# Kernel optimization log

Hardware: AMD Instinct MI355X
Metric: run time of the kernel (lower is better)

The kernel has to match this reference:

```python
import jax, jax.numpy as jnp
import numpy as np

N_NODES = 100000
N_EDGES = 1600000
F_IN = 128
F_OUT = 64


def setup_inputs() -> dict:
    key = jax.random.key(0)
    k0, k1, k2, k3, k4, k5 = jax.random.split(key, 6)
    stdv = 1.0 / np.sqrt(F_OUT)
    x = jax.random.normal(k0, (N_NODES, F_IN), dtype=jnp.float32)
    edge_src = jax.random.randint(k1, (N_EDGES,), 0, N_NODES, dtype=jnp.int32)
    edge_dst = jax.random.randint(k2, (N_EDGES,), 0, N_NODES, dtype=jnp.int32)
    # normalized adjacency values (all positive, like D^-1/2 A D^-1/2 entries)
    edge_weight = jax.random.uniform(k3, (N_EDGES,), dtype=jnp.float32)
    weight = jax.random.uniform(k4, (F_IN, F_OUT), dtype=jnp.float32, minval=-stdv, maxval=stdv)
    bias = jax.random.uniform(k5, (F_OUT,), dtype=jnp.float32, minval=-stdv, maxval=stdv)
    return {"x": x, "edge_weight": edge_weight, "weight": weight, "bias": bias,
            "edge_src": edge_src, "edge_dst": edge_dst}


def reference(x, edge_weight, weight, bias, edge_src, edge_dst):
    # support = X @ W  -- dense GEMM [N, F_in] x [F_in, F_out]
    support = x @ weight
    # spmm(adj, support): adj in COO form; gather source rows, scale by edge value,
    # scatter-add into destination rows.
    msgs = support[edge_src] * edge_weight[:, None]          # [E, F_out]
    out = jax.ops.segment_sum(msgs, edge_dst, num_segments=x.shape[0])
    return out + bias
```

## Files before the change

### kernel.cpp

```cpp
#include <hip/hip_runtime.h>
#include <hip/hip_bf16.h>

#define F_IN 128
#define F_OUT 64
#define BUCKET_SHIFT 7
#define BUCKET_NODES 128
#define BUCKET_CAP 2880
#define CNT_STRIDE 16
#define NB_MAX 800
#define SCAT_CHUNK 8192
#define GEMM_ROWS 64
#define LDK 136

typedef __attribute__((ext_vector_type(8))) short bf16x8;
typedef __attribute__((ext_vector_type(4))) float f32x4;

__device__ inline short bf16_bits(float f) {
  __hip_bfloat16 h = __float2bfloat16(f);
  return *reinterpret_cast<short*>(&h);
}

__global__ __launch_bounds__(256) void gcn_gemm_mfma_kernel(
    const float* __restrict__ x, const float* __restrict__ w,
    __hip_bfloat16* __restrict__ support, int n_nodes) {
  __shared__ short As[GEMM_ROWS][LDK];
  __shared__ short Bs[F_OUT][LDK];
  const int tid = threadIdx.x;
  const int block_row = blockIdx.x * GEMM_ROWS;

#pragma unroll
  for (int i = 0; i < F_IN * F_OUT / 256; ++i) {
    const int idx = tid + i * 256;
    const int k = idx >> 6;
    const int n = idx & 63;
    Bs[n][k] = bf16_bits(w[idx]);
  }
#pragma unroll
  for (int i = 0; i < GEMM_ROWS * F_IN / 4 / 256; ++i) {
    const int idx = tid + i * 256;
    const int row = idx >> 5;
    const int c4 = idx & 31;
    float4 v = make_float4(0.f, 0.f, 0.f, 0.f);
    if (block_row + row < n_nodes)
      v = ((const float4*)(x + (size_t)(block_row + row) * F_IN))[c4];
    short4 b;
    b.x = bf16_bits(v.x);
    b.y = bf16_bits(v.y);
    b.z = bf16_bits(v.z);
    b.w = bf16_bits(v.w);
    *(short4*)&As[row][c4 * 4] = b;
  }
  __syncthreads();

  const int lane = tid & 63;
  const int wid = tid >> 6;
  const int wr0 = wid * 16;
  const int m = lane & 15;
  const int quad = lane >> 4;

  f32x4 acc0 = {0.f, 0.f, 0.f, 0.f};
  f32x4 acc1 = {0.f, 0.f, 0.f, 0.f};
  f32x4 acc2 = {0.f, 0.f, 0.f, 0.f};
  f32x4 acc3 = {0.f, 0.f, 0.f, 0.f};
#pragma unroll
  for (int ks = 0; ks < 4; ++ks) {
    const int ko = ks * 32 + quad * 8;
    const bf16x8 a  = *(const bf16x8*)&As[wr0 + m][ko];
    const bf16x8 b0 = *(const bf16x8*)&Bs[0 + m][ko];
    const bf16x8 b1 = *(const bf16x8*)&Bs[16 + m][ko];
    const bf16x8 b2 = *(const bf16x8*)&Bs[32 + m][ko];
    const bf16x8 b3 = *(const bf16x8*)&Bs[48 + m][ko];
    acc0 = __builtin_amdgcn_mfma_f32_16x16x32_bf16(a, b0, acc0, 0, 0, 0);
    acc1 = __builtin_amdgcn_mfma_f32_16x16x32_bf16(a, b1, acc1, 0, 0, 0);
    acc2 = __builtin_amdgcn_mfma_f32_16x16x32_bf16(a, b2, acc2, 0, 0, 0);
    acc3 = __builtin_amdgcn_mfma_f32_16x16x32_bf16(a, b3, acc3, 0, 0, 0);
  }
#pragma unroll
  for (int r = 0; r < 4; ++r) {
    const int row = block_row + wr0 + quad * 4 + r;
    if (row < n_nodes) {
      __hip_bfloat16* op = support + (size_t)row * F_OUT;
      op[0 + m]  = __float2bfloat16(acc0[r]);
      op[16 + m] = __float2bfloat16(acc1[r]);
      op[32 + m] = __float2bfloat16(acc2[r]);
      op[48 + m] = __float2bfloat16(acc3[r]);
    }
  }
}

__global__ __launch_bounds__(512) void gcn_bucket_scatter_kernel(
    const int* __restrict__ esrc, const int* __restrict__ edst,
    const float* __restrict__ ew, int* __restrict__ bcount,
    int2* __restrict__ region, int n_edges, int nb) {
  __shared__ int lhist[NB_MAX];
  __shared__ int lcur[NB_MAX];
  __shared__ int ldst_cache[SCAT_CHUNK];
  const int e0 = blockIdx.x * SCAT_CHUNK;
  const int e1 = min(e0 + SCAT_CHUNK, n_edges);
  const int n_local = e1 - e0;

  for (int i = threadIdx.x; i < nb; i += 512) lhist[i] = 0;
  __syncthreads();
  for (int i = threadIdx.x; i < n_local; i += 512) {
    const int d = edst[e0 + i];
    ldst_cache[i] = d;
    atomicAdd(&lhist[d >> BUCKET_SHIFT], 1);
  }
  __syncthreads();
  for (int b = threadIdx.x; b < nb; b += 512) {
    const int c = lhist[b];
    lcur[b] = c ? atomicAdd(&bcount[b * CNT_STRIDE], c) : 0;
  }
  __syncthreads();
  for (int i = threadIdx.x; i < n_local; i += 512) {
    const int d = ldst_cache[i];
    const int b = d >> BUCKET_SHIFT;
    const int pos = atomicAdd(&lcur[b], 1);
    if (pos < BUCKET_CAP) {
      region[(size_t)b * BUCKET_CAP + pos] =
          make_int2((esrc[e0 + i] << BUCKET_SHIFT) | (d & (BUCKET_NODES - 1)),
                    __float_as_int(ew[e0 + i]));
    }
  }
}

__global__ __launch_bounds__(1024) void gcn_bucket_scan_kernel(
    const int* __restrict__ bcount, int* __restrict__ bbase, int nb) {
  __shared__ int wtot[16];
  const int lane = threadIdx.x & 63;
  const int wid = threadIdx.x >> 6;
  int c = 0;
  if (threadIdx.x < nb) {
    c = bcount[threadIdx.x * CNT_STRIDE];
    c = (c < BUCKET_CAP ? c : BUCKET_CAP);
  }
  int s = c;
#pragma unroll
  for (int off = 1; off < 64; off <<= 1) {
    const int t = __shfl_up(s, off, 64);
    if (lane >= off) s += t;
  }
  if (lane == 63) wtot[wid] = s;
  __syncthreads();
  if (wid == 0) {
    const int wv = (lane < 16) ? wtot[lane] : 0;
    int wsc = wv;
#pragma unroll
    for (int off = 1; off < 16; off <<= 1) {
      const int t = __shfl_up(wsc, off, 64);
      if (lane >= off) wsc += t;
    }
    if (lane < 16) wtot[lane] = wsc - wv;
  }
  __syncthreads();
  if (threadIdx.x < nb) bbase[threadIdx.x] = (s - c) + wtot[wid];
}

__global__ __launch_bounds__(256) void gcn_bucket_sort_kernel(
    const int2* __restrict__ region, const int* __restrict__ bcount,
    const int* __restrict__ bbase, int2* __restrict__ sorted,
    int* __restrict__ ends, int n_nodes) {
  __shared__ int2 eb[BUCKET_CAP];
  __shared__ int2 outb[BUCKET_CAP];
  __shared__ int lhist[BUCKET_NODES];
  __shared__ int lcur[BUCKET_NODES];
  const int b = blockIdx.x;
  int cnt = bcount[b * CNT_STRIDE];
  cnt = (cnt < BUCKET_CAP ? cnt : BUCKET_CAP);
  const int gbase = bbase[b];
  const int node0 = b << BUCKET_SHIFT;

  for (int i = threadIdx.x; i < BUCKET_NODES; i += 256) lhist[i] = 0;
  __syncthreads();
  for (int i = threadIdx.x; i < cnt; i += 256) {
    const int2 p = region[(size_t)b * BUCKET_CAP + i];
    eb[i] = p;
    atomicAdd(&lhist[p.x & (BUCKET_NODES - 1)], 1);
  }
  __syncthreads();
  const int lane = threadIdx.x & 63;
  if (threadIdx.x < 64) {
    const int v0 = lhist[lane];
    const int v1 = lhist[64 + lane];
    int s0 = v0;
#pragma unroll
    for (int off = 1; off < 64; off <<= 1) {
      const int t = __shfl_up(s0, off, 64);
      if (lane >= off) s0 += t;
    }
    const int tot0 = __shfl(s0, 63, 64);
    int s1 = v1;
#pragma unroll
    for (int off = 1; off < 64; off <<= 1) {
      const int t = __shfl_up(s1, off, 64);
      if (lane >= off) s1 += t;
    }
    s1 += tot0;
    lcur[lane] = s0 - v0;
    lcur[64 + lane] = s1 - v1;
    const int n0 = node0 + lane;
    const int n1 = node0 + 64 + lane;
    if (n0 < n_nodes) ends[n0] = gbase + s0;
    if (n1 < n_nodes) ends[n1] = gbase + s1;
  }
  __syncthreads();
  for (int i = threadIdx.x; i < cnt; i += 256) {
    const int2 p = eb[i];
    const int ldst = p.x & (BUCKET_NODES - 1);
    const int pos = atomicAdd(&lcur[ldst], 1);
    outb[pos] = make_int2(p.x >> BUCKET_SHIFT, p.y);
  }
  __syncthreads();
  for (int i = threadIdx.x; i < cnt; i += 256) {
    sorted[gbase + i] = outb[i];
  }
}

__global__ __launch_bounds__(256) void gcn_aggregate_kernel(
    const __hip_bfloat16* __restrict__ support, const int2* __restrict__ sorted,
    const int* __restrict__ ends, const float* __restrict__ bias,
    float* __restrict__ out, int n_nodes) {
  const int node = (blockIdx.x * 256 + threadIdx.x) >> 6;
  const int lane = threadIdx.x & 63;
  if (node >= n_nodes) return;
  const int start = (node == 0) ? 0 : ends[node - 1];
  const int end = ends[node];
  float acc = 0.f;
  for (int base = start; base < end; base += 64) {
    const int m = end - base;
    int2 meta = make_int2(0, 0);
    if (lane < m) meta = sorted[base + lane];
    const int m4 = (m < 64 ? m : 64);
    const int mr = (m4 + 7) & ~7;
    for (int j = 0; j < mr; j += 8) {
      int sidx[8];
      float wv[8];
#pragma unroll
      for (int u = 0; u < 8; ++u) {
        sidx[u] = __shfl(meta.x, j + u, 64);
        wv[u] = __int_as_float(__shfl(meta.y, j + u, 64));
      }
      float v[8];
#pragma unroll
      for (int u = 0; u < 8; ++u)
        v[u] = __bfloat162float(support[(size_t)sidx[u] * F_OUT + lane]);
#pragma unroll
      for (int u = 0; u < 8; ++u) acc += v[u] * wv[u];
    }
  }
  out[(size_t)node * F_OUT + lane] = acc + bias[lane];
}

extern "C" void kernel_launch(void* const* d_in, const int* in_sizes, int n_in,
                              void* d_out, int out_size, void* d_ws, size_t ws_size,
                              hipStream_t stream) {
  const float* x    = (const float*)d_in[0];
  const float* ew   = (const float*)d_in[1];
  const float* w    = (const float*)d_in[2];
  const float* bias = (const float*)d_in[3];
  const int*   esrc = (const int*)d_in[4];
  const int*   edst = (const int*)d_in[5];
  float* out = (float*)d_out;

  const int n_nodes = in_sizes[0] / F_IN;
  const int n_edges = in_sizes[4];
  const int nb = (n_nodes + BUCKET_NODES - 1) >> BUCKET_SHIFT;

  char* ws = (char*)d_ws;
  int2* sorted = (int2*)ws;
  ws += ((size_t)n_edges * sizeof(int2) + 255) / 256 * 256;
  int* ends = (int*)ws;
  ws += ((size_t)n_nodes * sizeof(int) + 255) / 256 * 256;
  int* bcount = (int*)ws;
  const size_t bcount_bytes = (size_t)nb * CNT_STRIDE * sizeof(int);
  ws += (bcount_bytes + 255) / 256 * 256;
  int* bbase = (int*)ws;
  ws += ((size_t)nb * sizeof(int) + 255) / 256 * 256;
  int2* region = (int2*)ws;
  __hip_bfloat16* support = (__hip_bfloat16*)ws;

  hipMemsetAsync(bcount, 0, bcount_bytes, stream);
  gcn_bucket_scatter_kernel<<<(n_edges + SCAT_CHUNK - 1) / SCAT_CHUNK, 512, 0,
                              stream>>>(esrc, edst, ew, bcount, region, n_edges,
                                        nb);
  gcn_bucket_scan_kernel<<<1, 1024, 0, stream>>>(bcount, bbase, nb);
  gcn_bucket_sort_kernel<<<nb, 256, 0, stream>>>(region, bcount, bbase, sorted,
                                                 ends, n_nodes);
  gcn_gemm_mfma_kernel<<<(n_nodes + GEMM_ROWS - 1) / GEMM_ROWS, 256, 0,
                         stream>>>(x, w, support, n_nodes);
  gcn_aggregate_kernel<<<(n_nodes * 64 + 255) / 256, 256, 0, stream>>>(
      support, sorted, ends, bias, out, n_nodes);
}
```

Measured before the change: 198.4 us.

## Fuse GEMM with bucket scatter, fold scan into sort, vectorize aggregate gathers

Merges the bucket-scatter and bf16 MFMA GEMM into one heterogeneous launch, with blocks branching on their id and sharing LDS through a union. GEMM tiles grow to 128 rows with 512 threads. The separate single-block scan kernel is removed, and each sort block now sums the counts of the preceding buckets itself. The aggregate kernel has each lane load 4 bf16 values for one of four edges at a time, then combines lanes with a cross-lane reduction and writes float4 outputs. This cuts launch count and serialization and uses wider gathers, at the cost of redundant prefix work in the sort and needing separate workspace for support when space allows.

```diff
diff --git a/kernel.cpp b/kernel.cpp
--- a/kernel.cpp
+++ b/kernel.cpp
@@ -9,7 +9,7 @@
 #define CNT_STRIDE 16
 #define NB_MAX 800
 #define SCAT_CHUNK 8192
-#define GEMM_ROWS 64
+#define P1_GEMM_ROWS 128
 #define LDK 136
 
 typedef __attribute__((ext_vector_type(8))) short bf16x8;
@@ -20,165 +20,146 @@
   return *reinterpret_cast<short*>(&h);
 }
 
-__global__ __launch_bounds__(256) void gcn_gemm_mfma_kernel(
+union Phase1Smem {
+  struct { short As[P1_GEMM_ROWS][LDK]; short Bs[F_OUT][LDK]; } g;
+  struct { int lhist[NB_MAX]; int lcur[NB_MAX]; int ldst[SCAT_CHUNK]; } s;
+};
+
+__global__ __launch_bounds__(512, 6) void gcn_phase1_kernel(
     const float* __restrict__ x, const float* __restrict__ w,
-    __hip_bfloat16* __restrict__ support, int n_nodes) {
-  __shared__ short As[GEMM_ROWS][LDK];
-  __shared__ short Bs[F_OUT][LDK];
-  const int tid = threadIdx.x;
-  const int block_row = blockIdx.x * GEMM_ROWS;
-
-#pragma unroll
-  for (int i = 0; i < F_IN * F_OUT / 256; ++i) {
-    const int idx = tid + i * 256;
-    const int k = idx >> 6;
-    const int n = idx & 63;
-    Bs[n][k] = bf16_bits(w[idx]);
-  }
-#pragma unroll
-  for (int i = 0; i < GEMM_ROWS * F_IN / 4 / 256; ++i) {
-    const int idx = tid + i * 256;
-    const int row = idx >> 5;
-    const int c4 = idx & 31;
-    float4 v = make_float4(0.f, 0.f, 0.f, 0.f);
-    if (block_row + row < n_nodes)
-      v = ((const float4*)(x + (size_t)(block_row + row) * F_IN))[c4];
-    short4 b;
-    b.x = bf16_bits(v.x);
-    b.y = bf16_bits(v.y);
-    b.z = bf16_bits(v.z);
-    b.w = bf16_bits(v.w);
-    *(short4*)&As[row][c4 * 4] = b;
-  }
-  __syncthreads();
-
-  const int lane = tid & 63;
-  const int wid = tid >> 6;
-  const int wr0 = wid * 16;
-  const int m = lane & 15;
-  const int quad = lane >> 4;
-
-  f32x4 acc0 = {0.f, 0.f, 0.f, 0.f};
-  f32x4 acc1 = {0.f, 0.f, 0.f, 0.f};
-  f32x4 acc2 = {0.f, 0.f, 0.f, 0.f};
-  f32x4 acc3 = {0.f, 0.f, 0.f, 0.f};
-#pragma unroll
-  for (int ks = 0; ks < 4; ++ks) {
-    const int ko = ks * 32 + quad * 8;
-    const bf16x8 a  = *(const bf16x8*)&As[wr0 + m][ko];
-    const bf16x8 b0 = *(const bf16x8*)&Bs[0 + m][ko];
-    const bf16x8 b1 = *(const bf16x8*)&Bs[16 + m][ko];
-    const bf16x8 b2 = *(const bf16x8*)&Bs[32 + m][ko];
-    const bf16x8 b3 = *(const bf16x8*)&Bs[48 + m][ko];
-    acc0 = __builtin_amdgcn_mfma_f32_16x16x32_bf16(a, b0, acc0, 0, 0, 0);
-    acc1 = __builtin_amdgcn_mfma_f32_16x16x32_bf16(a, b1, acc1, 0, 0, 0);
-    acc2 = __builtin_amdgcn_mfma_f32_16x16x32_bf16(a, b2, acc2, 0, 0, 0);
-    acc3 = __builtin_amdgcn_mfma_f32_16x16x32_bf16(a, b3, acc3, 0, 0, 0);
-  }
-#pragma unroll
-  for (int r = 0; r < 4; ++r) {
-    const int row = block_row + wr0 + quad * 4 + r;
-    if (row < n_nodes) {
-      __hip_bfloat16* op = support + (size_t)row * F_OUT;
-      op[0 + m]  = __float2bfloat16(acc0[r]);
-      op[16 + m] = __float2bfloat16(acc1[r]);
-      op[32 + m] = __float2bfloat16(acc2[r]);
-      op[48 + m] = __float2bfloat16(acc3[r]);
-    }
-  }
-}
-
-__global__ __launch_bounds__(512) void gcn_bucket_scatter_kernel(
+    __hip_bfloat16* __restrict__ support,
     const int* __restrict__ esrc, const int* __restrict__ edst,
     const float* __restrict__ ew, int* __restrict__ bcount,
-    int2* __restrict__ region, int n_edges, int nb) {
-  __shared__ int lhist[NB_MAX];
-  __shared__ int lcur[NB_MAX];
-  __shared__ int ldst_cache[SCAT_CHUNK];
-  const int e0 = blockIdx.x * SCAT_CHUNK;
-  const int e1 = min(e0 + SCAT_CHUNK, n_edges);
-  const int n_local = e1 - e0;
-
-  for (int i = threadIdx.x; i < nb; i += 512) lhist[i] = 0;
-  __syncthreads();
-  for (int i = threadIdx.x; i < n_local; i += 512) {
-    const int d = edst[e0 + i];
-    ldst_cache[i] = d;
-    atomicAdd(&lhist[d >> BUCKET_SHIFT], 1);
-  }
-  __syncthreads();
-  for (int b = threadIdx.x; b < nb; b += 512) {
-    const int c = lhist[b];
-    lcur[b] = c ? atomicAdd(&bcount[b * CNT_STRIDE], c) : 0;
-  }
-  __syncthreads();
-  for (int i = threadIdx.x; i < n_local; i += 512) {
-    const int d = ldst_cache[i];
-    const int b = d >> BUCKET_SHIFT;
-    const int pos = atomicAdd(&lcur[b], 1);
-    if (pos < BUCKET_CAP) {
-      region[(size_t)b * BUCKET_CAP + pos] =
-          make_int2((esrc[e0 + i] << BUCKET_SHIFT) | (d & (BUCKET_NODES - 1)),
-                    __float_as_int(ew[e0 + i]));
-    }
-  }
-}
-
-__global__ __launch_bounds__(1024) void gcn_bucket_scan_kernel(
-    const int* __restrict__ bcount, int* __restrict__ bbase, int nb) {
-  __shared__ int wtot[16];
-  const int lane = threadIdx.x & 63;
-  const int wid = threadIdx.x >> 6;
-  int c = 0;
-  if (threadIdx.x < nb) {
-    c = bcount[threadIdx.x * CNT_STRIDE];
-    c = (c < BUCKET_CAP ? c : BUCKET_CAP);
-  }
-  int s = c;
-#pragma unroll
-  for (int off = 1; off < 64; off <<= 1) {
-    const int t = __shfl_up(s, off, 64);
-    if (lane >= off) s += t;
-  }
-  if (lane == 63) wtot[wid] = s;
-  __syncthreads();
-  if (wid == 0) {
-    const int wv = (lane < 16) ? wtot[lane] : 0;
-    int wsc = wv;
-#pragma unroll
-    for (int off = 1; off < 16; off <<= 1) {
-      const int t = __shfl_up(wsc, off, 64);
-      if (lane >= off) wsc += t;
-    }
-    if (lane < 16) wtot[lane] = wsc - wv;
-  }
-  __syncthreads();
-  if (threadIdx.x < nb) bbase[threadIdx.x] = (s - c) + wtot[wid];
+    int2* __restrict__ region, int n_nodes, int n_edges, int nb,
+    int n_scat_blocks) {
+  __shared__ Phase1Smem sm;
+  const int tid = threadIdx.x;
+
+  if ((int)blockIdx.x < n_scat_blocks) {
+    const int e0 = blockIdx.x * SCAT_CHUNK;
+    const int e1 = min(e0 + SCAT_CHUNK, n_edges);
+    const int n_local = e1 - e0;
+
+    for (int i = tid; i < nb; i += 512) sm.s.lhist[i] = 0;
+    __syncthreads();
+    for (int i = tid; i < n_local; i += 512) {
+      const int d = edst[e0 + i];
+      sm.s.ldst[i] = d;
+      atomicAdd(&sm.s.lhist[d >> BUCKET_SHIFT], 1);
+    }
+    __syncthreads();
+    for (int b = tid; b < nb; b += 512) {
+      const int c = sm.s.lhist[b];
+      sm.s.lcur[b] = c ? atomicAdd(&bcount[b * CNT_STRIDE], c) : 0;
+    }
+    __syncthreads();
+    for (int i = tid; i < n_local; i += 512) {
+      const int d = sm.s.ldst[i];
+      const int b = d >> BUCKET_SHIFT;
+      const int pos = atomicAdd(&sm.s.lcur[b], 1);
+      if (pos < BUCKET_CAP) {
+        region[(size_t)b * BUCKET_CAP + pos] =
+            make_int2((esrc[e0 + i] << BUCKET_SHIFT) | (d & (BUCKET_NODES - 1)),
+                      __float_as_int(ew[e0 + i]));
+      }
+    }
+  } else {
+    const int gbid = (int)blockIdx.x - n_scat_blocks;
+    const int block_row = gbid * P1_GEMM_ROWS;
+
+#pragma unroll
+    for (int i = 0; i < F_IN * F_OUT / 512; ++i) {
+      const int idx = tid + i * 512;
+      sm.g.Bs[idx & 63][idx >> 6] = bf16_bits(w[idx]);
+    }
+#pragma unroll
+    for (int i = 0; i < P1_GEMM_ROWS * (F_IN / 4) / 512; ++i) {
+      const int idx = tid + i * 512;
+      const int row = idx >> 5;
+      const int c4 = idx & 31;
+      float4 v = make_float4(0.f, 0.f, 0.f, 0.f);
+      if (block_row + row < n_nodes)
+        v = ((const float4*)(x + (size_t)(block_row + row) * F_IN))[c4];
+      short4 b;
+      b.x = bf16_bits(v.x);
+      b.y = bf16_bits(v.y);
+      b.z = bf16_bits(v.z);
+      b.w = bf16_bits(v.w);
+      *(short4*)&sm.g.As[row][c4 * 4] = b;
+    }
+    __syncthreads();
+
+    const int lane = tid & 63;
+    const int wid = tid >> 6;
+    const int wr0 = wid * 16;
+    const int m = lane & 15;
+    const int quad = lane >> 4;
+
+    f32x4 acc0 = {0.f, 0.f, 0.f, 0.f};
+    f32x4 acc1 = {0.f, 0.f, 0.f, 0.f};
+    f32x4 acc2 = {0.f, 0.f, 0.f, 0.f};
+    f32x4 acc3 = {0.f, 0.f, 0.f, 0.f};
+#pragma unroll
+    for (int ks = 0; ks < 4; ++ks) {
+      const int ko = ks * 32 + quad * 8;
+      const bf16x8 a  = *(const bf16x8*)&sm.g.As[wr0 + m][ko];
+      const bf16x8 b0 = *(const bf16x8*)&sm.g.Bs[0 + m][ko];
+      const bf16x8 b1 = *(const bf16x8*)&sm.g.Bs[16 + m][ko];
+      const bf16x8 b2 = *(const bf16x8*)&sm.g.Bs[32 + m][ko];
+      const bf16x8 b3 = *(const bf16x8*)&sm.g.Bs[48 + m][ko];
+      acc0 = __builtin_amdgcn_mfma_f32_16x16x32_bf16(a, b0, acc0, 0, 0, 0);
+      acc1 = __builtin_amdgcn_mfma_f32_16x16x32_bf16(a, b1, acc1, 0, 0, 0);
+      acc2 = __builtin_amdgcn_mfma_f32_16x16x32_bf16(a, b2, acc2, 0, 0, 0);
+      acc3 = __builtin_amdgcn_mfma_f32_16x16x32_bf16(a, b3, acc3, 0, 0, 0);
+    }
+#pragma unroll
+    for (int r = 0; r < 4; ++r) {
+      const int row = block_row + wr0 + quad * 4 + r;
+      if (row < n_nodes) {
+        __hip_bfloat16* op = support + (size_t)row * F_OUT;
+        op[0 + m]  = __float2bfloat16(acc0[r]);
+        op[16 + m] = __float2bfloat16(acc1[r]);
+        op[32 + m] = __float2bfloat16(acc2[r]);
+        op[48 + m] = __float2bfloat16(acc3[r]);
+      }
+    }
+  }
 }
 
 __global__ __launch_bounds__(256) void gcn_bucket_sort_kernel(
     const int2* __restrict__ region, const int* __restrict__ bcount,
-    const int* __restrict__ bbase, int2* __restrict__ sorted,
-    int* __restrict__ ends, int n_nodes) {
+    int2* __restrict__ sorted, int* __restrict__ ends, int n_nodes, int nb) {
   __shared__ int2 eb[BUCKET_CAP];
   __shared__ int2 outb[BUCKET_CAP];
   __shared__ int lhist[BUCKET_NODES];
   __shared__ int lcur[BUCKET_NODES];
+  __shared__ int redw[4];
   const int b = blockIdx.x;
+  const int lane = threadIdx.x & 63;
+  const int wid = threadIdx.x >> 6;
+
+  int partial = 0;
+  for (int i = threadIdx.x; i < b; i += 256) {
+    const int cc = bcount[i * CNT_STRIDE];
+    partial += (cc < BUCKET_CAP ? cc : BUCKET_CAP);
+  }
+#pragma unroll
+  for (int off = 32; off >= 1; off >>= 1) partial += __shfl_xor(partial, off, 64);
+  if (lane == 0) redw[wid] = partial;
+  for (int i = threadIdx.x; i < BUCKET_NODES; i += 256) lhist[i] = 0;
+  __syncthreads();
+  const int gbase = redw[0] + redw[1] + redw[2] + redw[3];
+
   int cnt = bcount[b * CNT_STRIDE];
   cnt = (cnt < BUCKET_CAP ? cnt : BUCKET_CAP);
-  const int gbase = bbase[b];
   const int node0 = b << BUCKET_SHIFT;
 
-  for (int i = threadIdx.x; i < BUCKET_NODES; i += 256) lhist[i] = 0;
-  __syncthreads();
   for (int i = threadIdx.x; i < cnt; i += 256) {
     const int2 p = region[(size_t)b * BUCKET_CAP + i];
     eb[i] = p;
     atomicAdd(&lhist[p.x & (BUCKET_NODES - 1)], 1);
   }
   __syncthreads();
-  const int lane = threadIdx.x & 63;
   if (threadIdx.x < 64) {
     const int v0 = lhist[lane];
     const int v1 = lhist[64 + lane];
@@ -223,9 +204,14 @@
   const int node = (blockIdx.x * 256 + threadIdx.x) >> 6;
   const int lane = threadIdx.x & 63;
   if (node >= n_nodes) return;
+  const int r = lane >> 4;
+  const int c4 = (lane & 15) * 4;
   const int start = (node == 0) ? 0 : ends[node - 1];
   const int end = ends[node];
-  float acc = 0.f;
+  const ushort* sup = (const ushort*)support;
+
+  f32x4 acc0 = {0.f, 0.f, 0.f, 0.f};
+  f32x4 acc1 = {0.f, 0.f, 0.f, 0.f};
   for (int base = start; base < end; base += 64) {
     const int m = end - base;
     int2 meta = make_int2(0, 0);
@@ -233,22 +219,39 @@
     const int m4 = (m < 64 ? m : 64);
     const int mr = (m4 + 7) & ~7;
     for (int j = 0; j < mr; j += 8) {
-      int sidx[8];
-      float wv[8];
-#pragma unroll
-      for (int u = 0; u < 8; ++u) {
-        sidx[u] = __shfl(meta.x, j + u, 64);
-        wv[u] = __int_as_float(__shfl(meta.y, j + u, 64));
-      }
-      float v[8];
-#pragma unroll
-      for (int u = 0; u < 8; ++u)
-        v[u] = __bfloat162float(support[(size_t)sidx[u] * F_OUT + lane]);
-#pragma unroll
-      for (int u = 0; u < 8; ++u) acc += v[u] * wv[u];
-    }
-  }
-  out[(size_t)node * F_OUT + lane] = acc + bias[lane];
+      const int   s0 = __shfl(meta.x, j + r, 64);
+      const float w0 = __int_as_float(__shfl(meta.y, j + r, 64));
+      const int   s1 = __shfl(meta.x, j + 4 + r, 64);
+      const float w1 = __int_as_float(__shfl(meta.y, j + 4 + r, 64));
+      const uint2 d0 = *(const uint2*)(sup + (size_t)s0 * F_OUT + c4);
+      const uint2 d1 = *(const uint2*)(sup + (size_t)s1 * F_OUT + c4);
+      acc0[0] = fmaf(__uint_as_float(d0.x << 16), w0, acc0[0]);
+      acc0[1] = fmaf(__uint_as_float(d0.x & 0xffff0000u), w0, acc0[1]);
+      acc0[2] = fmaf(__uint_as_float(d0.y << 16), w0, acc0[2]);
+      acc0[3] = fmaf(__uint_as_float(d0.y & 0xffff0000u), w0, acc0[3]);
+      acc1[0] = fmaf(__uint_as_float(d1.x << 16), w1, acc1[0]);
+      acc1[1] = fmaf(__uint_as_float(d1.x & 0xffff0000u), w1, acc1[1]);
+      acc1[2] = fmaf(__uint_as_float(d1.y << 16), w1, acc1[2]);
+      acc1[3] = fmaf(__uint_as_float(d1.y & 0xffff0000u), w1, acc1[3]);
+    }
+  }
+  f32x4 acc;
+#pragma unroll
+  for (int i = 0; i < 4; ++i) {
+    float v = acc0[i] + acc1[i];
+    v += __shfl_xor(v, 16, 64);
+    v += __shfl_xor(v, 32, 64);
+    acc[i] = v;
+  }
+  if (r == 0) {
+    const float4 b4 = *(const float4*)(bias + c4);
+    float4 o;
+    o.x = acc[0] + b4.x;
+    o.y = acc[1] + b4.y;
+    o.z = acc[2] + b4.z;
+    o.w = acc[3] + b4.w;
+    *(float4*)(out + (size_t)node * F_OUT + c4) = o;
+  }
 }
 
 extern "C" void kernel_launch(void* const* d_in, const int* in_sizes, int n_in,
@@ -267,27 +270,47 @@
   const int nb = (n_nodes + BUCKET_NODES - 1) >> BUCKET_SHIFT;
 
   char* ws = (char*)d_ws;
-  int2* sorted = (int2*)ws;
-  ws += ((size_t)n_edges * sizeof(int2) + 255) / 256 * 256;
-  int* ends = (int*)ws;
-  ws += ((size_t)n_nodes * sizeof(int) + 255) / 256 * 256;
-  int* bcount = (int*)ws;
-  const size_t bcount_bytes = (size_t)nb * CNT_STRIDE * sizeof(int);
-  ws += (bcount_bytes + 255) / 256 * 256;
-  int* bbase = (int*)ws;
-  ws += ((size_t)nb * sizeof(int) + 255) / 256 * 256;
-  int2* region = (int2*)ws;
-  __hip_bfloat16* support = (__hip_bfloat16*)ws;
-
-  hipMemsetAsync(bcount, 0, bcount_bytes, stream);
-  gcn_bucket_scatter_kernel<<<(n_edges + SCAT_CHUNK - 1) / SCAT_CHUNK, 512, 0,
-                              stream>>>(esrc, edst, ew, bcount, region, n_edges,
-                                        nb);
-  gcn_bucket_scan_kernel<<<1, 1024, 0, stream>>>(bcount, bbase, nb);
-  gcn_bucket_sort_kernel<<<nb, 256, 0, stream>>>(region, bcount, bbase, sorted,
-                                                 ends, n_nodes);
-  gcn_gemm_mfma_kernel<<<(n_nodes + GEMM_ROWS - 1) / GEMM_ROWS, 256, 0,
-                         stream>>>(x, w, support, n_nodes);
-  gcn_aggregate_kernel<<<(n_nodes * 64 + 255) / 256, 256, 0, stream>>>(
-      support, sorted, ends, bias, out, n_nodes);
-}
+  size_t off = 0;
+  auto alloc = [&](size_t bytes) {
+    size_t o = off;
+    off += (bytes + 255) / 256 * 256;
+    return o;
+  };
+  const size_t off_sorted  = alloc((size_t)n_edges * sizeof(int2));
+  const size_t off_ends    = alloc((size_t)n_nodes * sizeof(int));
+  const size_t off_bcount  = alloc((size_t)nb * CNT_STRIDE * sizeof(int));
+  const size_t off_region  = alloc((size_t)nb * BUCKET_CAP * sizeof(int2));
+  const size_t off_support = off;
+  const size_t need_fused =
+      off_support + (size_t)n_nodes * F_OUT * sizeof(__hip_bfloat16);
+  const bool fused = (ws_size >= need_fused);
+
+  int2* sorted = (int2*)(ws + off_sorted);
+  int*  ends   = (int*)(ws + off_ends);
+  int*  bcount = (int*)(ws + off_bcount);
+  int2* region = (int2*)(ws + off_region);
+  __hip_bfloat16* support =
+      (__hip_bfloat16*)(ws + (fused ? off_support : off_region));
+
+  const int scat_blocks = (n_edges + SCAT_CHUNK - 1) / SCAT_CHUNK;
+  const int gemm_blocks = (n_nodes + P1_GEMM_ROWS - 1) / P1_GEMM_ROWS;
+
+  hipMemsetAsync(bcount, 0, (size_t)nb * CNT_STRIDE * sizeof(int), stream);
+  if (fused) {
+    gcn_phase1_kernel<<<scat_blocks + gemm_blocks, 512, 0, stream>>>(
+        x, w, support, esrc, edst, ew, bcount, region, n_nodes, n_edges, nb,
+        scat_blocks);
+    gcn_bucket_sort_kernel<<<nb, 256, 0, stream>>>(region, bcount, sorted,
+                                                   ends, n_nodes, nb);
+  } else {
+    gcn_phase1_kernel<<<scat_blocks, 512, 0, stream>>>(
+        x, w, support, esrc, edst, ew, bcount, region, n_nodes, n_edges, nb,
+        scat_blocks);
+    gcn_bucket_sort_kernel<<<nb, 256, 0, stream>>>(region, bcount, sorted,
+                                                   ends, n_nodes, nb);
+    gcn_phase1_kernel<<<gemm_blocks, 512, 0, stream>>>(
+        x, w, support, esrc, edst, ew, bcount, region, n_nodes, n_edges, nb, 0);
+  }
+  gcn_aggregate_kernel<<<(int)(((size_t)n_nodes * 64 + 255) / 256), 256, 0,
+                         stream>>>(support, sorted, ends, bias, out, n_nodes);
+}
```

After: 197.8 us. Within noise of the previous version (-0.3%).
